# Kernel optimization log

Hardware: AMD Instinct MI355X
Metric: run time of the kernel (lower is better)

The kernel has to match this reference:

```python
import jax, jax.numpy as jnp
import numpy as np

N = 4096            # nodes
LMAX = 6
NUM_COEF = (LMAX + 1) ** 2   # 49 SH coefficients
RES = 18            # S2 grid resolution (lat = lon = 18)
C = 128             # num_channels


def setup_inputs() -> dict:
    key = jax.random.key(0)
    k1, k2, k3, k4 = jax.random.split(key, 4)
    return {
        "inputs": jax.random.normal(k1, (N, NUM_COEF, 2 * C), dtype=jnp.float32),
        "scalars": jax.random.normal(k2, (N, 3 * C), dtype=jnp.float32),
        # SO3Grid projection matrices (precomputed SH-basis grids in the real module)
        "to_grid_mat": jax.random.normal(k3, (RES, RES, NUM_COEF), dtype=jnp.float32) / np.sqrt(NUM_COEF).astype(np.float32),
        "from_grid_mat": jax.random.normal(k4, (RES, RES, NUM_COEF), dtype=jnp.float32) / np.float32(RES),
    }


def reference(inputs, scalars, to_grid_mat, from_grid_mat):
    # inputs:  [N, (lmax+1)^2, 2C]; scalars: [N, 3C]
    n, k, c2 = inputs.shape
    s = scalars[:, None, :]                       # [N, 1, 3C]
    # Type-0 path part 1: SwiGLU on first 2C scalars -> [N, 1, C]
    a, b = jnp.split(s[..., :c2], 2, axis=-1)
    output_scalars = jax.nn.silu(a) * b
    # Type-0 path part 2: sigmoid gate on last C scalars -> [N, 1, C]
    gate_scalars = jax.nn.sigmoid(s[..., c2:])
    # Type-L path: project to S2 grid -> [N, RES, RES, 2C]
    x_grid = jnp.einsum('pqi,nic->npqc', to_grid_mat, inputs)
    # chunk-multiply gating (self tensor product) -> [N, RES, RES, C]
    x1, x2 = jnp.split(x_grid, 2, axis=-1)
    x_grid = x1 * x2
    # project back to SH coefficients -> [N, (lmax+1)^2, C]
    output_vectors = jnp.einsum('pqi,npqc->nic', from_grid_mat, x_grid)
    output_vectors = output_vectors * gate_scalars
    # merge: add SwiGLU scalars onto the l=0 component
    return output_vectors.at[:, 0:1, :].add(output_scalars)
```

## Files before the change

### kernel.cpp

```cpp
#include <hip/hip_runtime.h>


#define KC    49
#define PQ    324
#define NPX   12544
#define OUTK  6272
#define NTILE 11
#define TWROW  72
#define TWTILE 2304
#define TWTOT  25344
#define FWROW  40
#define FWTILE 2560
#define FWTOT  28160
#define WTOT   (TWTOT + FWTOT)

typedef __attribute__((ext_vector_type(8)))  short bf16x8;
typedef __attribute__((ext_vector_type(16))) float f32x16;
typedef __attribute__((ext_vector_type(4)))  unsigned int u32x4;

__device__ __forceinline__ unsigned int cvtpk_bf16(float lo, float hi) {
    unsigned int r;
    asm("v_cvt_pk_bf16_f32 %0, %1, %2" : "=v"(r) : "v"(lo), "v"(hi));
    return r;
}
__device__ __forceinline__ unsigned short f2bf(float f) {
    unsigned u = __builtin_bit_cast(unsigned, f);
    return (unsigned short)((u + 0x7FFFu + ((u >> 16) & 1u)) >> 16);
}

__global__ void prep_kernel(const float* __restrict__ Tg, const float* __restrict__ Fg,
                            unsigned short* __restrict__ W)
{
    const int idx = blockIdx.x * 256 + threadIdx.x;
    if (idx < TWTOT) {
        const int t = idx / TWTILE, rem = idx % TWTILE;
        const int r = rem / TWROW,  i   = rem % TWROW;
        const int pq = 32 * t + r;
        const float v = (i < KC && pq < PQ) ? Tg[pq * KC + i] : 0.0f;
        W[idx] = f2bf(v);
    } else if (idx < WTOT) {
        const int idx2 = idx - TWTOT;
        const int t = idx2 / FWTILE, rem = idx2 % FWTILE;
        const int k = rem / FWROW,   p   = rem % FWROW;
        const int pq = 32 * t + p;
        const float v = (k < KC && p < 32 && pq < PQ) ? Fg[pq * KC + k] : 0.0f;
        W[idx] = f2bf(v);
    }
}

__global__ __launch_bounds__(512, 2)
void s2_fused(const float* __restrict__ X,
              const float* __restrict__ S,
              const unsigned short* __restrict__ W,
              float* __restrict__ out,
              int nit)
{
    __shared__ __align__(16) unsigned short lds[WTOT];

    const int tid = threadIdx.x;
    for (int idx = tid; idx < WTOT / 8; idx += 512) {
        const u32x4 v = *(const u32x4*)(W + (size_t)idx * 8);
        *(u32x4*)(lds + (size_t)idx * 8) = v;
    }
    __syncthreads();

    const int w  = tid >> 6;
    const int l  = tid & 63;
    const int cl = l & 31;
    const int hb = l >> 5;
    const int cs = w >> 1;
    const int nw = w & 1;

    const unsigned short* tw = lds;
    const unsigned short* fw = lds + TWTOT;

    const int nbase = blockIdx.x * (2 * nit) + nw;

    float fr[2][4][8];
    float sraw0, sraw1, sraw2;

    {
        const float* xp = X + (size_t)nbase * NPX + 32 * cs + cl;
#pragma unroll
        for (int xi = 0; xi < 2; ++xi)
#pragma unroll
        for (int st = 0; st < 4; ++st)
#pragma unroll
        for (int j = 0; j < 8; ++j) {
            const int i = 16 * st + 8 * hb + j;
            fr[xi][st][j] = (i < KC) ? xp[128 * xi + (size_t)i * 256] : 0.0f;
        }
        const float* sp = S + (size_t)nbase * 384 + 32 * cs + cl;
        sraw0 = sp[0]; sraw1 = sp[128]; sraw2 = sp[256];
    }

    for (int it = 0; it < nit; ++it) {
        const int n = nbase + 2 * it;

        const float sg  = 1.0f / (1.0f + __expf(-sraw2));
        const float osc = (sraw0 / (1.0f + __expf(-sraw0))) * sraw1;

        bf16x8 bx[2][4];
#pragma unroll
        for (int xi = 0; xi < 2; ++xi)
#pragma unroll
        for (int st = 0; st < 4; ++st) {
            u32x4 d;
#pragma unroll
            for (int p = 0; p < 4; ++p)
                d[p] = cvtpk_bf16(fr[xi][st][2 * p], fr[xi][st][2 * p + 1]);
            bx[xi][st] = __builtin_bit_cast(bf16x8, d);
        }

        {
            const int n2 = nbase + 2 * ((it + 1 < nit) ? it + 1 : it);
            const float* xp = X + (size_t)n2 * NPX + 32 * cs + cl;
#pragma unroll
            for (int xi = 0; xi < 2; ++xi)
#pragma unroll
            for (int st = 0; st < 4; ++st)
#pragma unroll
            for (int j = 0; j < 8; ++j) {
                const int i = 16 * st + 8 * hb + j;
                fr[xi][st][j] = (i < KC) ? xp[128 * xi + (size_t)i * 256] : 0.0f;
            }
            const float* sp = S + (size_t)n2 * 384 + 32 * cs + cl;
            sraw0 = sp[0]; sraw1 = sp[128]; sraw2 = sp[256];
        }

        f32x16 accO0, accO1, fz;
#pragma unroll
        for (int r = 0; r < 16; ++r) { accO0[r] = 0.0f; accO1[r] = 0.0f; fz[r] = 0.0f; }

#pragma unroll 2
        for (int t = 0; t < NTILE; ++t) {
            const unsigned short* twt = tw + t * TWTILE + cl * TWROW + hb * 8;
            const bf16x8 ta0 = *(const bf16x8*)(twt);
            const bf16x8 ta1 = *(const bf16x8*)(twt + 16);
            const bf16x8 ta2 = *(const bf16x8*)(twt + 32);
            const bf16x8 ta3 = *(const bf16x8*)(twt + 48);
            const unsigned short* fwt = fw + t * FWTILE + cl * FWROW + hb * 8;
            const bf16x8 fa00 = *(const bf16x8*)(fwt);
            const bf16x8 fa01 = *(const bf16x8*)(fwt + 16);
            const bf16x8 fa10 = *(const bf16x8*)(fwt + 32 * FWROW);
            const bf16x8 fa11 = *(const bf16x8*)(fwt + 32 * FWROW + 16);

            f32x16 ac0 = fz, ac1 = fz;
            ac0 = __builtin_amdgcn_mfma_f32_32x32x16_bf16(ta0, bx[0][0], ac0, 0, 0, 0);
            ac1 = __builtin_amdgcn_mfma_f32_32x32x16_bf16(ta0, bx[1][0], ac1, 0, 0, 0);
            ac0 = __builtin_amdgcn_mfma_f32_32x32x16_bf16(ta1, bx[0][1], ac0, 0, 0, 0);
            ac1 = __builtin_amdgcn_mfma_f32_32x32x16_bf16(ta1, bx[1][1], ac1, 0, 0, 0);
            ac0 = __builtin_amdgcn_mfma_f32_32x32x16_bf16(ta2, bx[0][2], ac0, 0, 0, 0);
            ac1 = __builtin_amdgcn_mfma_f32_32x32x16_bf16(ta2, bx[1][2], ac1, 0, 0, 0);
            ac0 = __builtin_amdgcn_mfma_f32_32x32x16_bf16(ta3, bx[0][3], ac0, 0, 0, 0);
            ac1 = __builtin_amdgcn_mfma_f32_32x32x16_bf16(ta3, bx[1][3], ac1, 0, 0, 0);

            unsigned int q0 = cvtpk_bf16(ac0[0]  * ac1[0],  ac0[1]  * ac1[1]);
            unsigned int q1 = cvtpk_bf16(ac0[2]  * ac1[2],  ac0[3]  * ac1[3]);
            unsigned int q2 = cvtpk_bf16(ac0[4]  * ac1[4],  ac0[5]  * ac1[5]);
            unsigned int q3 = cvtpk_bf16(ac0[6]  * ac1[6],  ac0[7]  * ac1[7]);
            unsigned int q4 = cvtpk_bf16(ac0[8]  * ac1[8],  ac0[9]  * ac1[9]);
            unsigned int q5 = cvtpk_bf16(ac0[10] * ac1[10], ac0[11] * ac1[11]);
            unsigned int q6 = cvtpk_bf16(ac0[12] * ac1[12], ac0[13] * ac1[13]);
            unsigned int q7 = cvtpk_bf16(ac0[14] * ac1[14], ac0[15] * ac1[15]);

            asm("v_permlane32_swap_b32 %0, %1" : "+v"(q0), "+v"(q2));
            asm("v_permlane32_swap_b32 %0, %1" : "+v"(q1), "+v"(q3));
            asm("v_permlane32_swap_b32 %0, %1" : "+v"(q4), "+v"(q6));
            asm("v_permlane32_swap_b32 %0, %1" : "+v"(q5), "+v"(q7));
            u32x4 b0v, b1v;
            b0v[0] = q0; b0v[1] = q1; b0v[2] = q2; b0v[3] = q3;
            b1v[0] = q4; b1v[1] = q5; b1v[2] = q6; b1v[3] = q7;
            const bf16x8 bg0 = __builtin_bit_cast(bf16x8, b0v);
            const bf16x8 bg1 = __builtin_bit_cast(bf16x8, b1v);

            accO0 = __builtin_amdgcn_mfma_f32_32x32x16_bf16(fa00, bg0, accO0, 0, 0, 0);
            accO1 = __builtin_amdgcn_mfma_f32_32x32x16_bf16(fa10, bg0, accO1, 0, 0, 0);
            accO0 = __builtin_amdgcn_mfma_f32_32x32x16_bf16(fa01, bg1, accO0, 0, 0, 0);
            accO1 = __builtin_amdgcn_mfma_f32_32x32x16_bf16(fa11, bg1, accO1, 0, 0, 0);
        }

        float* op = out + (size_t)n * OUTK + 32 * cs + cl;
#pragma unroll
        for (int r = 0; r < 16; ++r) {
            const int k0 = (r & 3) + 8 * (r >> 2) + 4 * hb;
            float v = sg * accO0[r];
            if (k0 == 0) v += osc;
            op[(size_t)k0 * 128] = v;
            const int k1 = 32 + k0;
            if (k1 < KC) op[(size_t)k1 * 128] = sg * accO1[r];
        }
    }
}

extern "C" void kernel_launch(void* const* d_in, const int* in_sizes, int n_in,
                              void* d_out, int out_size, void* d_ws, size_t ws_size,
                              hipStream_t stream) {
    const float* inputs  = (const float*)d_in[0];
    const float* scalars = (const float*)d_in[1];
    const float* Tg      = (const float*)d_in[2];
    const float* Fg      = (const float*)d_in[3];
    float* outp          = (float*)d_out;

    unsigned short* W = (unsigned short*)d_ws;

    const int N = in_sizes[1] / 384;
    hipLaunchKernelGGL(prep_kernel, dim3((WTOT + 255) / 256), dim3(256), 0, stream,
                       Tg, Fg, W);

    const int nit  = 4;
    const int grid = N / (2 * nit);
    hipLaunchKernelGGL(s2_fused, dim3(grid), dim3(512), 0, stream,
                       inputs, scalars, W, outp, nit);
}
```

Before: 94.77 us.

## Process two nodes per wave per iteration to reuse LDS weight fragments

Each wave now handles two nodes per loop iteration, so every LDS-loaded weight fragment (to-grid and from-grid tiles) feeds MFMAs for both nodes, halving LDS reads per node. The register prefetch of the next node's inputs is dropped in favor of interleaved load/convert at the top of each iteration, and the grid is halved so each block covers 16 nodes. The cost is more accumulator registers, fewer blocks (256) on the device, and global loads no longer overlapped with the previous iteration's compute.

```diff
diff --git a/kernel.cpp b/kernel.cpp
--- a/kernel.cpp
+++ b/kernel.cpp
@@ -26,6 +26,19 @@
 __device__ __forceinline__ unsigned short f2bf(float f) {
     unsigned u = __builtin_bit_cast(unsigned, f);
     return (unsigned short)((u + 0x7FFFu + ((u >> 16) & 1u)) >> 16);
+}
+__device__ __forceinline__ void load_ch(const float* xp, int xi, int st, int hb, float* buf) {
+#pragma unroll
+    for (int j = 0; j < 8; ++j) {
+        const int i = 16 * st + 8 * hb + j;
+        buf[j] = (i < KC) ? xp[128 * xi + (size_t)i * 256] : 0.0f;
+    }
+}
+__device__ __forceinline__ bf16x8 cvt_ch(const float* buf) {
+    u32x4 d;
+#pragma unroll
+    for (int p = 0; p < 4; ++p) d[p] = cvtpk_bf16(buf[2 * p], buf[2 * p + 1]);
+    return __builtin_bit_cast(bf16x8, d);
 }
 
 __global__ void prep_kernel(const float* __restrict__ Tg, const float* __restrict__ Fg,
@@ -74,65 +87,55 @@
     const unsigned short* tw = lds;
     const unsigned short* fw = lds + TWTOT;
 
-    const int nbase = blockIdx.x * (2 * nit) + nw;
-
-    float fr[2][4][8];
-    float sraw0, sraw1, sraw2;
-
-    {
-        const float* xp = X + (size_t)nbase * NPX + 32 * cs + cl;
-#pragma unroll
-        for (int xi = 0; xi < 2; ++xi)
-#pragma unroll
-        for (int st = 0; st < 4; ++st)
-#pragma unroll
-        for (int j = 0; j < 8; ++j) {
-            const int i = 16 * st + 8 * hb + j;
-            fr[xi][st][j] = (i < KC) ? xp[128 * xi + (size_t)i * 256] : 0.0f;
-        }
-        const float* sp = S + (size_t)nbase * 384 + 32 * cs + cl;
-        sraw0 = sp[0]; sraw1 = sp[128]; sraw2 = sp[256];
-    }
-
     for (int it = 0; it < nit; ++it) {
-        const int n = nbase + 2 * it;
-
-        const float sg  = 1.0f / (1.0f + __expf(-sraw2));
-        const float osc = (sraw0 / (1.0f + __expf(-sraw0))) * sraw1;
-
-        bf16x8 bx[2][4];
-#pragma unroll
-        for (int xi = 0; xi < 2; ++xi)
-#pragma unroll
-        for (int st = 0; st < 4; ++st) {
-            u32x4 d;
-#pragma unroll
-            for (int p = 0; p < 4; ++p)
-                d[p] = cvtpk_bf16(fr[xi][st][2 * p], fr[xi][st][2 * p + 1]);
-            bx[xi][st] = __builtin_bit_cast(bf16x8, d);
-        }
-
-        {
-            const int n2 = nbase + 2 * ((it + 1 < nit) ? it + 1 : it);
-            const float* xp = X + (size_t)n2 * NPX + 32 * cs + cl;
-#pragma unroll
-            for (int xi = 0; xi < 2; ++xi)
-#pragma unroll
-            for (int st = 0; st < 4; ++st)
-#pragma unroll
-            for (int j = 0; j < 8; ++j) {
-                const int i = 16 * st + 8 * hb + j;
-                fr[xi][st][j] = (i < KC) ? xp[128 * xi + (size_t)i * 256] : 0.0f;
-            }
-            const float* sp = S + (size_t)n2 * 384 + 32 * cs + cl;
-            sraw0 = sp[0]; sraw1 = sp[128]; sraw2 = sp[256];
-        }
-
-        f32x16 accO0, accO1, fz;
-#pragma unroll
-        for (int r = 0; r < 16; ++r) { accO0[r] = 0.0f; accO1[r] = 0.0f; fz[r] = 0.0f; }
-
-#pragma unroll 2
+        const int base = blockIdx.x * (4 * nit) + 4 * it;
+        const int n0 = base + nw;
+        const int n1 = base + 2 + nw;
+
+        const float* sp0 = S + (size_t)n0 * 384 + 32 * cs + cl;
+        const float* sp1 = S + (size_t)n1 * 384 + 32 * cs + cl;
+        const float sg0  = 1.0f / (1.0f + __expf(-sp0[256]));
+        const float osc0 = (sp0[0] / (1.0f + __expf(-sp0[0]))) * sp0[128];
+        const float sg1  = 1.0f / (1.0f + __expf(-sp1[256]));
+        const float osc1 = (sp1[0] / (1.0f + __expf(-sp1[0]))) * sp1[128];
+
+        bf16x8 bx0[2][4], bx1[2][4];
+        {
+            const float* xp0 = X + (size_t)n0 * NPX + 32 * cs + cl;
+            float rA[8], rB[8];
+            load_ch(xp0, 0, 0, hb, rA);
+            load_ch(xp0, 1, 0, hb, rB);
+            bx0[0][0] = cvt_ch(rA); load_ch(xp0, 0, 1, hb, rA);
+            bx0[1][0] = cvt_ch(rB); load_ch(xp0, 1, 1, hb, rB);
+            bx0[0][1] = cvt_ch(rA); load_ch(xp0, 0, 2, hb, rA);
+            bx0[1][1] = cvt_ch(rB); load_ch(xp0, 1, 2, hb, rB);
+            bx0[0][2] = cvt_ch(rA); load_ch(xp0, 0, 3, hb, rA);
+            bx0[1][2] = cvt_ch(rB); load_ch(xp0, 1, 3, hb, rB);
+            bx0[0][3] = cvt_ch(rA);
+            bx0[1][3] = cvt_ch(rB);
+        }
+        {
+            const float* xp1 = X + (size_t)n1 * NPX + 32 * cs + cl;
+            float rA[8], rB[8];
+            load_ch(xp1, 0, 0, hb, rA);
+            load_ch(xp1, 1, 0, hb, rB);
+            bx1[0][0] = cvt_ch(rA); load_ch(xp1, 0, 1, hb, rA);
+            bx1[1][0] = cvt_ch(rB); load_ch(xp1, 1, 1, hb, rB);
+            bx1[0][1] = cvt_ch(rA); load_ch(xp1, 0, 2, hb, rA);
+            bx1[1][1] = cvt_ch(rB); load_ch(xp1, 1, 2, hb, rB);
+            bx1[0][2] = cvt_ch(rA); load_ch(xp1, 0, 3, hb, rA);
+            bx1[1][2] = cvt_ch(rB); load_ch(xp1, 1, 3, hb, rB);
+            bx1[0][3] = cvt_ch(rA);
+            bx1[1][3] = cvt_ch(rB);
+        }
+
+        f32x16 accO00, accO01, accO10, accO11;
+#pragma unroll
+        for (int r = 0; r < 16; ++r) {
+            accO00[r] = 0.0f; accO01[r] = 0.0f;
+            accO10[r] = 0.0f; accO11[r] = 0.0f;
+        }
+
         for (int t = 0; t < NTILE; ++t) {
             const unsigned short* twt = tw + t * TWTILE + cl * TWROW + hb * 8;
             const bf16x8 ta0 = *(const bf16x8*)(twt);
@@ -145,50 +148,78 @@
             const bf16x8 fa10 = *(const bf16x8*)(fwt + 32 * FWROW);
             const bf16x8 fa11 = *(const bf16x8*)(fwt + 32 * FWROW + 16);
 
-            f32x16 ac0 = fz, ac1 = fz;
-            ac0 = __builtin_amdgcn_mfma_f32_32x32x16_bf16(ta0, bx[0][0], ac0, 0, 0, 0);
-            ac1 = __builtin_amdgcn_mfma_f32_32x32x16_bf16(ta0, bx[1][0], ac1, 0, 0, 0);
-            ac0 = __builtin_amdgcn_mfma_f32_32x32x16_bf16(ta1, bx[0][1], ac0, 0, 0, 0);
-            ac1 = __builtin_amdgcn_mfma_f32_32x32x16_bf16(ta1, bx[1][1], ac1, 0, 0, 0);
-            ac0 = __builtin_amdgcn_mfma_f32_32x32x16_bf16(ta2, bx[0][2], ac0, 0, 0, 0);
-            ac1 = __builtin_amdgcn_mfma_f32_32x32x16_bf16(ta2, bx[1][2], ac1, 0, 0, 0);
-            ac0 = __builtin_amdgcn_mfma_f32_32x32x16_bf16(ta3, bx[0][3], ac0, 0, 0, 0);
-            ac1 = __builtin_amdgcn_mfma_f32_32x32x16_bf16(ta3, bx[1][3], ac1, 0, 0, 0);
-
-            unsigned int q0 = cvtpk_bf16(ac0[0]  * ac1[0],  ac0[1]  * ac1[1]);
-            unsigned int q1 = cvtpk_bf16(ac0[2]  * ac1[2],  ac0[3]  * ac1[3]);
-            unsigned int q2 = cvtpk_bf16(ac0[4]  * ac1[4],  ac0[5]  * ac1[5]);
-            unsigned int q3 = cvtpk_bf16(ac0[6]  * ac1[6],  ac0[7]  * ac1[7]);
-            unsigned int q4 = cvtpk_bf16(ac0[8]  * ac1[8],  ac0[9]  * ac1[9]);
-            unsigned int q5 = cvtpk_bf16(ac0[10] * ac1[10], ac0[11] * ac1[11]);
-            unsigned int q6 = cvtpk_bf16(ac0[12] * ac1[12], ac0[13] * ac1[13]);
-            unsigned int q7 = cvtpk_bf16(ac0[14] * ac1[14], ac0[15] * ac1[15]);
-
-            asm("v_permlane32_swap_b32 %0, %1" : "+v"(q0), "+v"(q2));
-            asm("v_permlane32_swap_b32 %0, %1" : "+v"(q1), "+v"(q3));
-            asm("v_permlane32_swap_b32 %0, %1" : "+v"(q4), "+v"(q6));
-            asm("v_permlane32_swap_b32 %0, %1" : "+v"(q5), "+v"(q7));
-            u32x4 b0v, b1v;
-            b0v[0] = q0; b0v[1] = q1; b0v[2] = q2; b0v[3] = q3;
-            b1v[0] = q4; b1v[1] = q5; b1v[2] = q6; b1v[3] = q7;
-            const bf16x8 bg0 = __builtin_bit_cast(bf16x8, b0v);
-            const bf16x8 bg1 = __builtin_bit_cast(bf16x8, b1v);
-
-            accO0 = __builtin_amdgcn_mfma_f32_32x32x16_bf16(fa00, bg0, accO0, 0, 0, 0);
-            accO1 = __builtin_amdgcn_mfma_f32_32x32x16_bf16(fa10, bg0, accO1, 0, 0, 0);
-            accO0 = __builtin_amdgcn_mfma_f32_32x32x16_bf16(fa01, bg1, accO0, 0, 0, 0);
-            accO1 = __builtin_amdgcn_mfma_f32_32x32x16_bf16(fa11, bg1, accO1, 0, 0, 0);
-        }
-
-        float* op = out + (size_t)n * OUTK + 32 * cs + cl;
-#pragma unroll
-        for (int r = 0; r < 16; ++r) {
-            const int k0 = (r & 3) + 8 * (r >> 2) + 4 * hb;
-            float v = sg * accO0[r];
-            if (k0 == 0) v += osc;
-            op[(size_t)k0 * 128] = v;
-            const int k1 = 32 + k0;
-            if (k1 < KC) op[(size_t)k1 * 128] = sg * accO1[r];
+#pragma unroll
+            for (int ni = 0; ni < 2; ++ni) {
+                const bf16x8 (*bx)[4] = ni ? bx1 : bx0;
+
+                f32x16 ac0, ac1;
+#pragma unroll
+                for (int r = 0; r < 16; ++r) { ac0[r] = 0.0f; ac1[r] = 0.0f; }
+                ac0 = __builtin_amdgcn_mfma_f32_32x32x16_bf16(ta0, bx[0][0], ac0, 0, 0, 0);
+                ac1 = __builtin_amdgcn_mfma_f32_32x32x16_bf16(ta0, bx[1][0], ac1, 0, 0, 0);
+                ac0 = __builtin_amdgcn_mfma_f32_32x32x16_bf16(ta1, bx[0][1], ac0, 0, 0, 0);
+                ac1 = __builtin_amdgcn_mfma_f32_32x32x16_bf16(ta1, bx[1][1], ac1, 0, 0, 0);
+                ac0 = __builtin_amdgcn_mfma_f32_32x32x16_bf16(ta2, bx[0][2], ac0, 0, 0, 0);
+                ac1 = __builtin_amdgcn_mfma_f32_32x32x16_bf16(ta2, bx[1][2], ac1, 0, 0, 0);
+                ac0 = __builtin_amdgcn_mfma_f32_32x32x16_bf16(ta3, bx[0][3], ac0, 0, 0, 0);
+                ac1 = __builtin_amdgcn_mfma_f32_32x32x16_bf16(ta3, bx[1][3], ac1, 0, 0, 0);
+
+                unsigned int q0 = cvtpk_bf16(ac0[0]  * ac1[0],  ac0[1]  * ac1[1]);
+                unsigned int q1 = cvtpk_bf16(ac0[2]  * ac1[2],  ac0[3]  * ac1[3]);
+                unsigned int q2 = cvtpk_bf16(ac0[4]  * ac1[4],  ac0[5]  * ac1[5]);
+                unsigned int q3 = cvtpk_bf16(ac0[6]  * ac1[6],  ac0[7]  * ac1[7]);
+                unsigned int q4 = cvtpk_bf16(ac0[8]  * ac1[8],  ac0[9]  * ac1[9]);
+                unsigned int q5 = cvtpk_bf16(ac0[10] * ac1[10], ac0[11] * ac1[11]);
+                unsigned int q6 = cvtpk_bf16(ac0[12] * ac1[12], ac0[13] * ac1[13]);
+                unsigned int q7 = cvtpk_bf16(ac0[14] * ac1[14], ac0[15] * ac1[15]);
+
+                asm("v_permlane32_swap_b32 %0, %1" : "+v"(q0), "+v"(q2));
+                asm("v_permlane32_swap_b32 %0, %1" : "+v"(q1), "+v"(q3));
+                asm("v_permlane32_swap_b32 %0, %1" : "+v"(q4), "+v"(q6));
+                asm("v_permlane32_swap_b32 %0, %1" : "+v"(q5), "+v"(q7));
+                u32x4 b0v, b1v;
+                b0v[0] = q0; b0v[1] = q1; b0v[2] = q2; b0v[3] = q3;
+                b1v[0] = q4; b1v[1] = q5; b1v[2] = q6; b1v[3] = q7;
+                const bf16x8 bg0 = __builtin_bit_cast(bf16x8, b0v);
+                const bf16x8 bg1 = __builtin_bit_cast(bf16x8, b1v);
+
+                if (ni == 0) {
+                    accO00 = __builtin_amdgcn_mfma_f32_32x32x16_bf16(fa00, bg0, accO00, 0, 0, 0);
+                    accO01 = __builtin_amdgcn_mfma_f32_32x32x16_bf16(fa10, bg0, accO01, 0, 0, 0);
+                    accO00 = __builtin_amdgcn_mfma_f32_32x32x16_bf16(fa01, bg1, accO00, 0, 0, 0);
+                    accO01 = __builtin_amdgcn_mfma_f32_32x32x16_bf16(fa11, bg1, accO01, 0, 0, 0);
+                } else {
+                    accO10 = __builtin_amdgcn_mfma_f32_32x32x16_bf16(fa00, bg0, accO10, 0, 0, 0);
+                    accO11 = __builtin_amdgcn_mfma_f32_32x32x16_bf16(fa10, bg0, accO11, 0, 0, 0);
+                    accO10 = __builtin_amdgcn_mfma_f32_32x32x16_bf16(fa01, bg1, accO10, 0, 0, 0);
+                    accO11 = __builtin_amdgcn_mfma_f32_32x32x16_bf16(fa11, bg1, accO11, 0, 0, 0);
+                }
+            }
+        }
+
+        {
+            float* op = out + (size_t)n0 * OUTK + 32 * cs + cl;
+#pragma unroll
+            for (int r = 0; r < 16; ++r) {
+                const int k0 = (r & 3) + 8 * (r >> 2) + 4 * hb;
+                float v = sg0 * accO00[r];
+                if (k0 == 0) v += osc0;
+                op[(size_t)k0 * 128] = v;
+                const int k1 = 32 + k0;
+                if (k1 < KC) op[(size_t)k1 * 128] = sg0 * accO01[r];
+            }
+        }
+        {
+            float* op = out + (size_t)n1 * OUTK + 32 * cs + cl;
+#pragma unroll
+            for (int r = 0; r < 16; ++r) {
+                const int k0 = (r & 3) + 8 * (r >> 2) + 4 * hb;
+                float v = sg1 * accO10[r];
+                if (k0 == 0) v += osc1;
+                op[(size_t)k0 * 128] = v;
+                const int k1 = 32 + k0;
+                if (k1 < KC) op[(size_t)k1 * 128] = sg1 * accO11[r];
+            }
         }
     }
 }
@@ -209,7 +240,7 @@
                        Tg, Fg, W);
 
     const int nit  = 4;
-    const int grid = N / (2 * nit);
+    const int grid = N / (4 * nit);
     hipLaunchKernelGGL(s2_fused, dim3(grid), dim3(512), 0, stream,
                        inputs, scalars, W, outp, nit);
 }
```

Result: slower. 112.5 us (+18.8%).
